# Kernel tuning notes

Hardware: AMD Instinct MI355X
Metric: run time of the kernel (lower is better)

## Reference

```python
import jax, jax.numpy as jnp
import numpy as np

D_STATE = 16

def setup_inputs() -> dict:
    key = jax.random.key(0)
    ks = jax.random.split(key, 7)
    B, L, d_model = 2, 4096, 1024
    d_inner, d_conv, d_state = 2048, 4, D_STATE
    s = 0.02
    return {
        "x": jax.random.normal(ks[0], (B, L, d_model), jnp.float32),
        "W_in": jax.random.normal(ks[1], (2 * d_inner, d_model), jnp.float32) * s,
        "conv_w": jax.random.normal(ks[2], (d_inner, d_conv), jnp.float32) * 0.3,
        "conv_b": jax.random.normal(ks[3], (d_inner,), jnp.float32) * 0.1,
        "W_xproj": jax.random.normal(ks[4], (2 * d_state + d_inner, d_inner), jnp.float32) * s,
        "D": jnp.ones((d_inner,), jnp.float32),
        "W_out": jax.random.normal(ks[5], (d_model, d_inner), jnp.float32) * s,
    }

def _silu(v):
    return v * jax.nn.sigmoid(v)

def reference(x, W_in, conv_w, conv_b, W_xproj, D, W_out):
    Bsz, L, _ = x.shape
    d_inner, d_conv = conv_w.shape
    d_state = D_STATE
    # in_proj -> split into x branch and gate z
    xz = jnp.einsum('bld,ed->ble', x, W_in)           # [B,L,2*d_inner]
    xb, z = xz[..., :d_inner], xz[..., d_inner:]
    # causal depthwise conv1d (left pad d_conv-1, truncate to L)
    xpad = jnp.pad(xb, ((0, 0), (d_conv - 1, 0), (0, 0)))
    xc = conv_b
    for k in range(d_conv):  # tiny fixed kernel loop
        xc = xc + conv_w[:, k] * xpad[:, k:k + L, :]
    xc = _silu(xc)                                    # [B,L,d_inner]
    # x_proj -> B, C, delta
    proj = jnp.einsum('bld,ed->ble', xc, W_xproj)     # [B,L,2*d_state+d_inner]
    Bm = proj[..., :d_state]
    Cm = proj[..., d_state:2 * d_state]
    delta = jax.nn.softplus(proj[..., 2 * d_state:])  # [B,L,d_inner]
    # selective 'scan' as written collapses: y[b,l,d] = delta*x * sum_s B*C + D*x
    bc = jnp.einsum('bls,bls->bl', Bm, Cm)            # [B,L]
    y = delta * xc * bc[..., None] + D * xc
    y = y * _silu(z)
    return jnp.einsum('bld,ed->ble', y, W_out)        # [B,L,d_model]
```

## Files before the change

### kernel.cpp

```cpp
#include <hip/hip_runtime.h>
#include <hip/hip_bf16.h>
#include <cstdint>
#include <cmath>

typedef __bf16 bf16x8 __attribute__((ext_vector_type(8)));
typedef float  f32x4  __attribute__((ext_vector_type(4)));
typedef unsigned short u16x8 __attribute__((ext_vector_type(8)));

#define BT 128
#define BK 64

__device__ __forceinline__ float bf2f(unsigned short h) {
  union { unsigned int u; float f; } v; v.u = ((unsigned int)h) << 16;
  return v.f;
}
__device__ __forceinline__ unsigned short f2bf(float x) {
  union { float f; unsigned int u; } v; v.f = x;
  unsigned int r = v.u + 0x7fffu + ((v.u >> 16) & 1u);
  return (unsigned short)(r >> 16);
}

__device__ __forceinline__ void gld_lds16(const void* g, void* l) {
  __builtin_amdgcn_global_load_lds(
      (const __attribute__((address_space(1))) unsigned int*)g,
      (__attribute__((address_space(3))) unsigned int*)l,
      16, 0, 0);
}

__device__ __forceinline__ void cvt4(const float* __restrict__ in,
                                     unsigned short* __restrict__ out, int i) {
  float4 v = reinterpret_cast<const float4*>(in)[i];
  ushort4 o;
  o.x = f2bf(v.x); o.y = f2bf(v.y); o.z = f2bf(v.z); o.w = f2bf(v.w);
  reinterpret_cast<ushort4*>(out)[i] = o;
}

__global__ void cvt_head(const float* __restrict__ x, unsigned short* __restrict__ xb,
                         const float* __restrict__ W_in, unsigned short* __restrict__ wb) {
  int b = blockIdx.x;
  if (b < 8192) cvt4(x, xb, b * 256 + threadIdx.x);
  else          cvt4(W_in, wb, (b - 8192) * 256 + threadIdx.x);
}

__device__ void conv_strip(const unsigned short* __restrict__ xz,
                           const float* __restrict__ conv_w,
                           const float* __restrict__ conv_b,
                           unsigned short* __restrict__ xc,
                           int strip, int tid) {
  const int bl0  = strip * 32;
  const int seq0 = bl0 & ~4095;
  const int c0   = tid * 8;
  float w[4][8], bb[8];
#pragma unroll
  for (int j = 0; j < 8; ++j) {
    float4 wr = reinterpret_cast<const float4*>(conv_w)[c0 + j];
    w[0][j] = wr.x; w[1][j] = wr.y; w[2][j] = wr.z; w[3][j] = wr.w;
    bb[j] = conv_b[c0 + j];
  }
  float win[3][8];
#pragma unroll
  for (int i = 0; i < 3; ++i) {
    int r = bl0 - 3 + i;
    if (r >= seq0) {
      u16x8 v = *reinterpret_cast<const u16x8*>(xz + (size_t)r * 4096 + c0);
#pragma unroll
      for (int j = 0; j < 8; ++j) win[i][j] = bf2f(v[j]);
    } else {
#pragma unroll
      for (int j = 0; j < 8; ++j) win[i][j] = 0.f;
    }
  }
  for (int i = 0; i < 32; ++i) {
    const int bl = bl0 + i;
    u16x8 v = *reinterpret_cast<const u16x8*>(xz + (size_t)bl * 4096 + c0);
    u16x8 o;
#pragma unroll
    for (int j = 0; j < 8; ++j) {
      float cur = bf2f(v[j]);
      float a = bb[j] + w[0][j] * win[0][j] + w[1][j] * win[1][j]
                      + w[2][j] * win[2][j] + w[3][j] * cur;
      o[j] = f2bf(a / (1.f + __expf(-a)));
      win[0][j] = win[1][j]; win[1][j] = win[2][j]; win[2][j] = cur;
    }
    *reinterpret_cast<u16x8*>(xc + (size_t)bl * 2048 + c0) = o;
  }
}

__global__ void mid_fused(const unsigned short* __restrict__ xz,
                          const float* __restrict__ conv_w,
                          const float* __restrict__ conv_b,
                          unsigned short* __restrict__ xc,
                          const float* __restrict__ W_xproj, unsigned short* __restrict__ wx_bf,
                          const float* __restrict__ W_out,   unsigned short* __restrict__ wo_bf) {
  int b = blockIdx.x;
  if (b < 256) { conv_strip(xz, conv_w, conv_b, xc, b, threadIdx.x); return; }
  b -= 256;
  if (b < 4160) { cvt4(W_xproj, wx_bf, b * 256 + threadIdx.x); return; }
  cvt4(W_out, wo_bf, (b - 4160) * 256 + threadIdx.x);
}

template <int GUARD_N, int OUT_F32>
__global__ __launch_bounds__(256, 2)
void gemm_bt(const unsigned short* __restrict__ A,
             const unsigned short* __restrict__ B,
             void* __restrict__ Cv,
             int N, int K, int ldA, int ldB, int ldC)
{
  __shared__ __align__(16) unsigned short sA[BT * BK];
  __shared__ __align__(16) unsigned short sB[BT * BK];

  const int tid  = threadIdx.x;
  const int lane = tid & 63;
  const int wave = tid >> 6;
  const int row0 = blockIdx.x * BT;
  const int col0 = blockIdx.y * BT;

  const int wrow = (wave & 1) * 64;
  const int wcol = (wave >> 1) * 64;
  const int l15  = lane & 15;
  const int q    = lane >> 4;

  f32x4 acc[4][4];
#pragma unroll
  for (int i = 0; i < 4; ++i)
#pragma unroll
    for (int j = 0; j < 4; ++j)
      acc[i][j] = (f32x4){0.f, 0.f, 0.f, 0.f};

  const int nk = K / BK;
  for (int kt = 0; kt < nk; ++kt) {
    const int k0 = kt * BK;
#pragma unroll
    for (int t = 0; t < 4; ++t) {
      int c  = t * 256 + tid;
      int r  = c >> 3;
      int g  = c & 7;
      int gs = (g ^ (r & 7)) * 8;
      gld_lds16(A + (size_t)(row0 + r) * ldA + k0 + gs, (void*)(sA + c * 8));
      int br = col0 + r;
      if (GUARD_N) br = (br < N) ? br : (N - 1);
      gld_lds16(B + (size_t)br * ldB + k0 + gs, (void*)(sB + c * 8));
    }
    __syncthreads();

#pragma unroll
    for (int kk = 0; kk < BK; kk += 32) {
      const int grb = kk >> 3;
      bf16x8 af[4], bfr[4];
#pragma unroll
      for (int i = 0; i < 4; ++i) {
        int ar = wrow + i * 16 + l15;
        af[i] = *reinterpret_cast<const bf16x8*>(
            sA + ar * BK + (((grb + q) ^ (ar & 7)) << 3));
        int br = wcol + i * 16 + l15;
        bfr[i] = *reinterpret_cast<const bf16x8*>(
            sB + br * BK + (((grb + q) ^ (br & 7)) << 3));
      }
#pragma unroll
      for (int i = 0; i < 4; ++i)
#pragma unroll
        for (int j = 0; j < 4; ++j)
          acc[i][j] = __builtin_amdgcn_mfma_f32_16x16x32_bf16(af[i], bfr[j], acc[i][j], 0, 0, 0);
    }
    __syncthreads();
  }

#pragma unroll
  for (int i = 0; i < 4; ++i) {
#pragma unroll
    for (int j = 0; j < 4; ++j) {
      int colw = col0 + wcol + j * 16 + l15;
      if (GUARD_N && colw >= N) continue;
#pragma unroll
      for (int r = 0; r < 4; ++r) {
        int roww = row0 + wrow + i * 16 + q * 4 + r;
        if (OUT_F32)
          ((float*)Cv)[(size_t)roww * ldC + colw] = acc[i][j][r];
        else
          ((unsigned short*)Cv)[(size_t)roww * ldC + colw] = f2bf(acc[i][j][r]);
      }
    }
  }
}

#define BARX() do { __builtin_amdgcn_sched_barrier(0); \
                    __builtin_amdgcn_s_barrier(); \
                    __builtin_amdgcn_sched_barrier(0); } while (0)
#define VMW(n) asm volatile("s_waitcnt vmcnt(" #n ")" ::: "memory")
#define LGKM0() asm volatile("s_waitcnt lgkmcnt(0)" ::: "memory")

#define STAGE_A(b, h, kt) do { \
  const unsigned short* _p = Ab + (size_t)((h) * 128) * ldA + (kt) * 64; \
  gld_lds16(_p,                     (void*)&sA[b][((h) * 128      + rr) * 64 + (g8 << 3)]); \
  gld_lds16(_p + (size_t)64 * ldA,  (void*)&sA[b][((h) * 128 + 64 + rr) * 64 + (g8 << 3)]); \
} while (0)

#define STAGE_B(b, h, kt) do { \
  const unsigned short* _p = Bb + (size_t)((h) * 128) * ldB + (kt) * 64; \
  gld_lds16(_p,                     (void*)&sB[b][((h) * 128      + rr) * 64 + (g8 << 3)]); \
  gld_lds16(_p + (size_t)64 * ldB,  (void*)&sB[b][((h) * 128 + 64 + rr) * 64 + (g8 << 3)]); \
} while (0)

#define RD_A_SET(dst, b, p) do { \
  dst[0][0] = *reinterpret_cast<const bf16x8*>(&sA[b][aOff + (2*(p)    ) * 1024 + kph0]); \
  dst[0][1] = *reinterpret_cast<const bf16x8*>(&sA[b][aOff + (2*(p)    ) * 1024 + kph1]); \
  dst[1][0] = *reinterpret_cast<const bf16x8*>(&sA[b][aOff + (2*(p) + 1) * 1024 + kph0]); \
  dst[1][1] = *reinterpret_cast<const bf16x8*>(&sA[b][aOff + (2*(p) + 1) * 1024 + kph1]); \
} while (0)

#define RD_B_SET(dst, b) do { \
  dst[0][0] = *reinterpret_cast<const bf16x8*>(&sB[b][bOff + 0 * 1024 + kph0]); \
  dst[0][1] = *reinterpret_cast<const bf16x8*>(&sB[b][bOff + 0 * 1024 + kph1]); \
  dst[1][0] = *reinterpret_cast<const bf16x8*>(&sB[b][bOff + 1 * 1024 + kph0]); \
  dst[1][1] = *reinterpret_cast<const bf16x8*>(&sB[b][bOff + 1 * 1024 + kph1]); \
  dst[2][0] = *reinterpret_cast<const bf16x8*>(&sB[b][bOff + 2 * 1024 + kph0]); \
  dst[2][1] = *reinterpret_cast<const bf16x8*>(&sB[b][bOff + 2 * 1024 + kph1]); \
  dst[3][0] = *reinterpret_cast<const bf16x8*>(&sB[b][bOff + 3 * 1024 + kph0]); \
  dst[3][1] = *reinterpret_cast<const bf16x8*>(&sB[b][bOff + 3 * 1024 + kph1]); \
} while (0)

#define MMA(i, j, k, Af, Bf) \
  acc[i][j] = __builtin_amdgcn_mfma_f32_16x16x32_bf16(Af[(i) & 1][k], Bf[j][k], acc[i][j], 0, 0, 0)

#define MFMA_PH(p, Af, Bf) do { \
  __builtin_amdgcn_s_setprio(1); \
  MMA(2*(p),   0, 0, Af, Bf); MMA(2*(p),   1, 0, Af, Bf); \
  MMA(2*(p),   2, 0, Af, Bf); MMA(2*(p),   3, 0, Af, Bf); \
  MMA(2*(p)+1, 0, 0, Af, Bf); MMA(2*(p)+1, 1, 0, Af, Bf); \
  MMA(2*(p)+1, 2, 0, Af, Bf); MMA(2*(p)+1, 3, 0, Af, Bf); \
  MMA(2*(p),   0, 1, Af, Bf); MMA(2*(p),   1, 1, Af, Bf); \
  MMA(2*(p),   2, 1, Af, Bf); MMA(2*(p),   3, 1, Af, Bf); \
  MMA(2*(p)+1, 0, 1, Af, Bf); MMA(2*(p)+1, 1, 1, Af, Bf); \
  MMA(2*(p)+1, 2, 1, Af, Bf); MMA(2*(p)+1, 3, 1, Af, Bf); \
  __builtin_amdgcn_s_setprio(0); \
} while (0)

__global__ __launch_bounds__(512, 2)
void gemm256(const unsigned short* __restrict__ A,
             const unsigned short* __restrict__ B,
             unsigned short* __restrict__ C,
             int K, int ldA, int ldB, int ldC, int ccsh)
{
  __shared__ __align__(16) unsigned short smem[4 * 256 * 64];
  unsigned short (*sA)[256 * 64] = (unsigned short (*)[256 * 64])smem;
  unsigned short (*sB)[256 * 64] = (unsigned short (*)[256 * 64])(smem + 2 * 256 * 64);

  const int tid  = threadIdx.x;
  const int lane = tid & 63;
  const int wave = tid >> 6;
  const int wm = wave >> 2;
  const int wn = wave & 3;
  const int l15 = lane & 15;
  const int q   = lane >> 4;

  const int nwg = gridDim.x;
  const int wg  = blockIdx.x;
  const int x   = wg & 7;
  const int c   = wg >> 3;
  const int CC  = 1 << ccsh;
  const int R   = (nwg >> 3) >> ccsh;
  const int row0 = ((x >> 1) * R + (c >> ccsh)) * 256;
  const int col0 = ((x & 1) * CC + (c & (CC - 1))) * 256;

  const int rr  = tid >> 3;
  const int g8  = tid & 7;
  const int gsw = ((g8 ^ (rr & 7)) << 3);
  const unsigned short* Ab = A + (size_t)(row0 + rr) * ldA + gsw;
  const unsigned short* Bb = B + (size_t)(col0 + rr) * ldB + gsw;

  const int aOff = (wm * 128 + l15) * 64;
  const int bOff = (wn * 64  + l15) * 64;
  const int a7   = l15 & 7;
  const int kph0 = ((q       ^ a7) << 3);
  const int kph1 = (((4 + q) ^ a7) << 3);

  f32x4 acc[8][4];
#pragma unroll
  for (int i = 0; i < 8; ++i)
#pragma unroll
    for (int j = 0; j < 4; ++j)
      acc[i][j] = (f32x4){0.f, 0.f, 0.f, 0.f};

  bf16x8 afe[2][2], afo[2][2];
  bf16x8 bfe[4][2], bfo[4][2];

  const int nk = K >> 6;
  STAGE_A(0, 0, 0); STAGE_A(0, 1, 0);
  STAGE_B(0, 0, 0); STAGE_B(0, 1, 0);
  STAGE_B(1, 0, 1); STAGE_B(1, 1, 1);
  VMW(4);
  BARX();
  RD_B_SET(bfe, 0); RD_A_SET(afe, 0, 0);

  const int niter = K >> 7;
  for (int it = 0; it < niter; ++it) {
    const int kt1 = 2 * it + 1;
    int ktE = 2 * it + 2; if (ktE > nk - 1) ktE = nk - 1;
    int ktO = 2 * it + 3; if (ktO > nk - 1) ktO = nk - 1;

    STAGE_A(1, 0, kt1);
    BARX();
    MFMA_PH(0, afe, bfe); RD_A_SET(afo, 0, 1);
    BARX();
    STAGE_A(1, 1, kt1);
    BARX();
    MFMA_PH(1, afo, bfe); RD_A_SET(afe, 0, 2);
    BARX();
    STAGE_B(0, 0, ktE);
    BARX();
    MFMA_PH(2, afe, bfe); RD_A_SET(afo, 0, 3);
    BARX();
    STAGE_B(0, 1, ktE);
    VMW(4);
    BARX();
    MFMA_PH(3, afo, bfe); RD_B_SET(bfo, 1); RD_A_SET(afe, 1, 0);
    BARX();

    STAGE_A(0, 0, ktE);
    BARX();
    MFMA_PH(0, afe, bfo); RD_A_SET(afo, 1, 1);
    BARX();
    STAGE_A(0, 1, ktE);
    BARX();
    MFMA_PH(1, afo, bfo); RD_A_SET(afe, 1, 2);
    BARX();
    STAGE_B(1, 0, ktO);
    BARX();
    MFMA_PH(2, afe, bfo); RD_A_SET(afo, 1, 3);
    BARX();
    STAGE_B(1, 1, ktO);
    VMW(4);
    BARX();
    MFMA_PH(3, afo, bfo); RD_B_SET(bfe, 0); RD_A_SET(afe, 0, 0);
    BARX();
  }

  VMW(0);
  LGKM0();
  BARX();
  {
    unsigned short* cs = smem;
#pragma unroll
    for (int i = 0; i < 8; ++i) {
      const int row = wm * 128 + i * 16 + q * 4;
#pragma unroll
      for (int j = 0; j < 4; ++j) {
        const int col = (wn * 64 + j * 16 + l15) ^ (q << 4);
#pragma unroll
        for (int r = 0; r < 4; ++r)
          cs[(row + r) * 256 + col] = f2bf(acc[i][j][r]);
      }
    }
    LGKM0();
    BARX();
#pragma unroll
    for (int s = 0; s < 16; ++s) {
      const int u   = s * 4096 + tid * 8;
      const int row = u >> 8;
      const int col = u & 255;
      const int rcol = col ^ (((row >> 2) & 3) << 4);
      u16x8 v = *reinterpret_cast<const u16x8*>(&cs[row * 256 + rcol]);
      *reinterpret_cast<u16x8*>(C + (size_t)(row0 + row) * ldC + col0 + col) = v;
    }
  }
}

__global__ __launch_bounds__(256)
void proj_strip(const unsigned short* __restrict__ xc,
                const unsigned short* __restrict__ wx,
                unsigned short* __restrict__ proj)
{
  __shared__ float red[4][32 * 32];
  const int tid  = threadIdx.x;
  const int lane = tid & 63;
  const int wave = tid >> 6;
  const int l15  = lane & 15;
  const int q    = lane >> 4;
  const int row0 = blockIdx.x * 32;

  f32x4 acc[2][2];
#pragma unroll
  for (int i = 0; i < 2; ++i)
#pragma unroll
    for (int j = 0; j < 2; ++j) acc[i][j] = (f32x4){0.f, 0.f, 0.f, 0.f};

  const int kbase = wave * 512;
#pragma unroll 4
  for (int kk = 0; kk < 512; kk += 32) {
    const int k = kbase + kk + q * 8;
    bf16x8 a0 = *reinterpret_cast<const bf16x8*>(&xc[(size_t)(row0 + l15) * 2048 + k]);
    bf16x8 a1 = *reinterpret_cast<const bf16x8*>(&xc[(size_t)(row0 + 16 + l15) * 2048 + k]);
    bf16x8 b0 = *reinterpret_cast<const bf16x8*>(&wx[(size_t)(l15) * 2048 + k]);
    bf16x8 b1 = *reinterpret_cast<const bf16x8*>(&wx[(size_t)(16 + l15) * 2048 + k]);
    acc[0][0] = __builtin_amdgcn_mfma_f32_16x16x32_bf16(a0, b0, acc[0][0], 0, 0, 0);
    acc[0][1] = __builtin_amdgcn_mfma_f32_16x16x32_bf16(a0, b1, acc[0][1], 0, 0, 0);
    acc[1][0] = __builtin_amdgcn_mfma_f32_16x16x32_bf16(a1, b0, acc[1][0], 0, 0, 0);
    acc[1][1] = __builtin_amdgcn_mfma_f32_16x16x32_bf16(a1, b1, acc[1][1], 0, 0, 0);
  }

#pragma unroll
  for (int i = 0; i < 2; ++i)
#pragma unroll
    for (int j = 0; j < 2; ++j)
#pragma unroll
      for (int r = 0; r < 4; ++r)
        red[wave][(i * 16 + q * 4 + r) * 32 + j * 16 + l15] = acc[i][j][r];
  __syncthreads();

#pragma unroll
  for (int t = 0; t < 4; ++t) {
    int idx = tid + t * 256;
    float s = red[0][idx] + red[1][idx] + red[2][idx] + red[3][idx];
    proj[(size_t)(row0 + (idx >> 5)) * 2080 + (idx & 31)] = f2bf(s);
  }
}

__global__ void gate_kernel(const unsigned short* __restrict__ proj,
                            const unsigned short* __restrict__ xz,
                            const float* __restrict__ Dw,
                            unsigned short* __restrict__ xc_y)
{
  const int bl = blockIdx.x;
  const unsigned short* p = proj + (size_t)bl * 2080;
  u16x8 pb0 = *reinterpret_cast<const u16x8*>(p);
  u16x8 pb1 = *reinterpret_cast<const u16x8*>(p + 8);
  u16x8 pc0 = *reinterpret_cast<const u16x8*>(p + 16);
  u16x8 pc1 = *reinterpret_cast<const u16x8*>(p + 24);
  float bc = 0.f;
#pragma unroll
  for (int s = 0; s < 8; ++s)
    bc += bf2f(pb0[s]) * bf2f(pc0[s]) + bf2f(pb1[s]) * bf2f(pc1[s]);

  const int c0 = threadIdx.x * 8;
  u16x8 dv  = *reinterpret_cast<const u16x8*>(p + 32 + c0);
  u16x8 xcv = *reinterpret_cast<const u16x8*>(xc_y + (size_t)bl * 2048 + c0);
  u16x8 zv  = *reinterpret_cast<const u16x8*>(xz + (size_t)bl * 4096 + 2048 + c0);
  float4 d0 = reinterpret_cast<const float4*>(Dw)[c0 / 4];
  float4 d1 = reinterpret_cast<const float4*>(Dw)[c0 / 4 + 1];
  const float* dd0 = reinterpret_cast<const float*>(&d0);
  const float* dd1 = reinterpret_cast<const float*>(&d1);

  u16x8 o;
#pragma unroll
  for (int j = 0; j < 8; ++j) {
    float d = bf2f(dv[j]);
    float delta = (d > 15.f) ? d : __logf(1.f + __expf(d));
    float xv = bf2f(xcv[j]);
    float z  = bf2f(zv[j]);
    float Dj = (j < 4) ? dd0[j] : dd1[j - 4];
    float y = delta * xv * bc + Dj * xv;
    y *= z / (1.f + __expf(-z));
    o[j] = f2bf(y);
  }
  *reinterpret_cast<u16x8*>(xc_y + (size_t)bl * 2048 + c0) = o;
}

extern "C" void kernel_launch(void* const* d_in, const int* in_sizes, int n_in,
                              void* d_out, int out_size, void* d_ws, size_t ws_size,
                              hipStream_t stream) {
  const float* x       = (const float*)d_in[0];
  const float* W_in    = (const float*)d_in[1];
  const float* conv_w  = (const float*)d_in[2];
  const float* conv_b  = (const float*)d_in[3];
  const float* W_xproj = (const float*)d_in[4];
  const float* Dw      = (const float*)d_in[5];
  const float* W_out   = (const float*)d_in[6];
  float* out = (float*)d_out;

  unsigned short* xz_bf   = (unsigned short*)d_ws;
  unsigned short* xc_bf   = xz_bf  + (size_t)8192 * 4096;
  unsigned short* proj_bf = xc_bf  + (size_t)8192 * 2048;
  unsigned short* xb_bf   = proj_bf + (size_t)8192 * 2080;
  unsigned short* w_bf    = xb_bf  + (size_t)8192 * 1024;

  cvt_head<<<8192 + 4096, 256, 0, stream>>>(x, xb_bf, W_in, w_bf);
  gemm256<<<512, 512, 0, stream>>>(xb_bf, w_bf, xz_bf, 1024, 1024, 1024, 4096, 3);
  mid_fused<<<256 + 4160 + 2048, 256, 0, stream>>>(xz_bf, conv_w, conv_b, xc_bf,
                                                   W_xproj, xb_bf, W_out, w_bf);
  proj_strip<<<256, 256, 0, stream>>>(xc_bf, xb_bf, proj_bf);
  gemm256<<<256, 512, 0, stream>>>(xc_bf, xb_bf + (size_t)32 * 2048, proj_bf + 32,
                                   2048, 2048, 2048, 2080, 2);
  gate_kernel<<<8192, 256, 0, stream>>>(proj_bf, xz_bf, Dw, xc_bf);
  gemm_bt<0, 1><<<dim3(64, 8), 256, 0, stream>>>(xc_bf, w_bf, out, 1024, 2048, 2048, 2048, 1024);
}
```

Before: 346.3 us.

## Fuse gating epilogue into delta GEMM and reduce B·C inside proj_strip

The elementwise gating kernel is removed. The delta GEMM now computes softplus, the D skip term and the SiLU(z) gate in its epilogue, writing y directly to a new buffer. proj_strip now reduces B·C per row to a single float instead of writing the B and C columns of proj. This drops one kernel launch and the round trip of the full delta matrix through memory, at the cost of a heavier GEMM epilogue that also loads xc, z and bc.

```diff
diff --git a/kernel.cpp b/kernel.cpp
--- a/kernel.cpp
+++ b/kernel.cpp
@@ -235,11 +235,15 @@
   __builtin_amdgcn_s_setprio(0); \
 } while (0)
 
+template <int EPI>
 __global__ __launch_bounds__(512, 2)
 void gemm256(const unsigned short* __restrict__ A,
              const unsigned short* __restrict__ B,
              unsigned short* __restrict__ C,
-             int K, int ldA, int ldB, int ldC, int ccsh)
+             int K, int ldA, int ldB, int ldC, int ccsh,
+             const unsigned short* __restrict__ XZ,
+             const float* __restrict__ Dw,
+             const float* __restrict__ BC)
 {
   __shared__ __align__(16) unsigned short smem[4 * 256 * 64];
   unsigned short (*sA)[256 * 64] = (unsigned short (*)[256 * 64])smem;
@@ -353,14 +357,48 @@
     }
     LGKM0();
     BARX();
-#pragma unroll
-    for (int s = 0; s < 16; ++s) {
-      const int u   = s * 4096 + tid * 8;
-      const int row = u >> 8;
-      const int col = u & 255;
-      const int rcol = col ^ (((row >> 2) & 3) << 4);
-      u16x8 v = *reinterpret_cast<const u16x8*>(&cs[row * 256 + rcol]);
-      *reinterpret_cast<u16x8*>(C + (size_t)(row0 + row) * ldC + col0 + col) = v;
+
+    const int colf   = (tid * 8) & 255;
+    const int rowofs = tid >> 5;
+
+    if (EPI == 0) {
+#pragma unroll
+      for (int s = 0; s < 16; ++s) {
+        const int row  = s * 16 + rowofs;
+        const int rcol = colf ^ (((row >> 2) & 3) << 4);
+        u16x8 v = *reinterpret_cast<const u16x8*>(&cs[row * 256 + rcol]);
+        *reinterpret_cast<u16x8*>(C + (size_t)(row0 + row) * ldC + col0 + colf) = v;
+      }
+    } else {
+      float dj[8];
+      {
+        float4 d0 = reinterpret_cast<const float4*>(Dw)[(col0 + colf) >> 2];
+        float4 d1 = reinterpret_cast<const float4*>(Dw)[((col0 + colf) >> 2) + 1];
+        dj[0] = d0.x; dj[1] = d0.y; dj[2] = d0.z; dj[3] = d0.w;
+        dj[4] = d1.x; dj[5] = d1.y; dj[6] = d1.z; dj[7] = d1.w;
+      }
+#pragma unroll
+      for (int s = 0; s < 16; ++s) {
+        const int row  = s * 16 + rowofs;
+        const int rcol = colf ^ (((row >> 2) & 3) << 4);
+        const size_t gr = (size_t)(row0 + row);
+        u16x8 pv  = *reinterpret_cast<const u16x8*>(&cs[row * 256 + rcol]);
+        u16x8 xcv = *reinterpret_cast<const u16x8*>(A + gr * ldA + col0 + colf);
+        u16x8 zv  = *reinterpret_cast<const u16x8*>(XZ + gr * 4096 + 2048 + col0 + colf);
+        const float bcr = BC[gr];
+        u16x8 o;
+#pragma unroll
+        for (int j = 0; j < 8; ++j) {
+          float p  = bf2f(pv[j]);
+          float delta = (p > 15.f) ? p : __logf(1.f + __expf(p));
+          float xv = bf2f(xcv[j]);
+          float zz = bf2f(zv[j]);
+          float y  = delta * xv * bcr + dj[j] * xv;
+          y *= zz / (1.f + __expf(-zz));
+          o[j] = f2bf(y);
+        }
+        *reinterpret_cast<u16x8*>(C + gr * ldC + col0 + colf) = o;
+      }
     }
   }
 }
@@ -368,9 +406,9 @@
 __global__ __launch_bounds__(256)
 void proj_strip(const unsigned short* __restrict__ xc,
                 const unsigned short* __restrict__ wx,
-                unsigned short* __restrict__ proj)
+                float* __restrict__ bc)
 {
-  __shared__ float red[4][32 * 32];
+  __shared__ float red[4][32 * 33];
   const int tid  = threadIdx.x;
   const int lane = tid & 63;
   const int wave = tid >> 6;
@@ -404,55 +442,20 @@
     for (int j = 0; j < 2; ++j)
 #pragma unroll
       for (int r = 0; r < 4; ++r)
-        red[wave][(i * 16 + q * 4 + r) * 32 + j * 16 + l15] = acc[i][j][r];
+        red[wave][(i * 16 + q * 4 + r) * 33 + j * 16 + l15] = acc[i][j][r];
   __syncthreads();
 
-#pragma unroll
-  for (int t = 0; t < 4; ++t) {
-    int idx = tid + t * 256;
-    float s = red[0][idx] + red[1][idx] + red[2][idx] + red[3][idx];
-    proj[(size_t)(row0 + (idx >> 5)) * 2080 + (idx & 31)] = f2bf(s);
-  }
-}
-
-__global__ void gate_kernel(const unsigned short* __restrict__ proj,
-                            const unsigned short* __restrict__ xz,
-                            const float* __restrict__ Dw,
-                            unsigned short* __restrict__ xc_y)
-{
-  const int bl = blockIdx.x;
-  const unsigned short* p = proj + (size_t)bl * 2080;
-  u16x8 pb0 = *reinterpret_cast<const u16x8*>(p);
-  u16x8 pb1 = *reinterpret_cast<const u16x8*>(p + 8);
-  u16x8 pc0 = *reinterpret_cast<const u16x8*>(p + 16);
-  u16x8 pc1 = *reinterpret_cast<const u16x8*>(p + 24);
-  float bc = 0.f;
-#pragma unroll
-  for (int s = 0; s < 8; ++s)
-    bc += bf2f(pb0[s]) * bf2f(pc0[s]) + bf2f(pb1[s]) * bf2f(pc1[s]);
-
-  const int c0 = threadIdx.x * 8;
-  u16x8 dv  = *reinterpret_cast<const u16x8*>(p + 32 + c0);
-  u16x8 xcv = *reinterpret_cast<const u16x8*>(xc_y + (size_t)bl * 2048 + c0);
-  u16x8 zv  = *reinterpret_cast<const u16x8*>(xz + (size_t)bl * 4096 + 2048 + c0);
-  float4 d0 = reinterpret_cast<const float4*>(Dw)[c0 / 4];
-  float4 d1 = reinterpret_cast<const float4*>(Dw)[c0 / 4 + 1];
-  const float* dd0 = reinterpret_cast<const float*>(&d0);
-  const float* dd1 = reinterpret_cast<const float*>(&d1);
-
-  u16x8 o;
-#pragma unroll
-  for (int j = 0; j < 8; ++j) {
-    float d = bf2f(dv[j]);
-    float delta = (d > 15.f) ? d : __logf(1.f + __expf(d));
-    float xv = bf2f(xcv[j]);
-    float z  = bf2f(zv[j]);
-    float Dj = (j < 4) ? dd0[j] : dd1[j - 4];
-    float y = delta * xv * bc + Dj * xv;
-    y *= z / (1.f + __expf(-z));
-    o[j] = f2bf(y);
-  }
-  *reinterpret_cast<u16x8*>(xc_y + (size_t)bl * 2048 + c0) = o;
+  if (tid < 32) {
+    float s = 0.f;
+#pragma unroll
+    for (int cc = 0; cc < 16; ++cc) {
+      const int ib = tid * 33 + cc;
+      float b  = red[0][ib] + red[1][ib] + red[2][ib] + red[3][ib];
+      float cv = red[0][ib + 16] + red[1][ib + 16] + red[2][ib + 16] + red[3][ib + 16];
+      s += b * cv;
+    }
+    bc[row0 + tid] = s;
+  }
 }
 
 extern "C" void kernel_launch(void* const* d_in, const int* in_sizes, int n_in,
@@ -469,17 +472,19 @@
 
   unsigned short* xz_bf   = (unsigned short*)d_ws;
   unsigned short* xc_bf   = xz_bf  + (size_t)8192 * 4096;
-  unsigned short* proj_bf = xc_bf  + (size_t)8192 * 2048;
-  unsigned short* xb_bf   = proj_bf + (size_t)8192 * 2080;
+  unsigned short* y_bf    = xc_bf  + (size_t)8192 * 2048;
+  float*          bc_ws   = (float*)(y_bf + (size_t)8192 * 2048);
+  unsigned short* xb_bf   = y_bf + (size_t)8192 * 2080;
   unsigned short* w_bf    = xb_bf  + (size_t)8192 * 1024;
 
   cvt_head<<<8192 + 4096, 256, 0, stream>>>(x, xb_bf, W_in, w_bf);
-  gemm256<<<512, 512, 0, stream>>>(xb_bf, w_bf, xz_bf, 1024, 1024, 1024, 4096, 3);
+  gemm256<0><<<512, 512, 0, stream>>>(xb_bf, w_bf, xz_bf, 1024, 1024, 1024, 4096, 3,
+                                      nullptr, nullptr, nullptr);
   mid_fused<<<256 + 4160 + 2048, 256, 0, stream>>>(xz_bf, conv_w, conv_b, xc_bf,
                                                    W_xproj, xb_bf, W_out, w_bf);
-  proj_strip<<<256, 256, 0, stream>>>(xc_bf, xb_bf, proj_bf);
-  gemm256<<<256, 512, 0, stream>>>(xc_bf, xb_bf + (size_t)32 * 2048, proj_bf + 32,
-                                   2048, 2048, 2048, 2080, 2);
-  gate_kernel<<<8192, 256, 0, stream>>>(proj_bf, xz_bf, Dw, xc_bf);
-  gemm_bt<0, 1><<<dim3(64, 8), 256, 0, stream>>>(xc_bf, w_bf, out, 1024, 2048, 2048, 2048, 1024);
-}
+  proj_strip<<<256, 256, 0, stream>>>(xc_bf, xb_bf, bc_ws);
+  gemm256<1><<<256, 512, 0, stream>>>(xc_bf, xb_bf + (size_t)32 * 2048, y_bf,
+                                      2048, 2048, 2048, 2048, 2,
+                                      xz_bf, Dw, bc_ws);
+  gemm_bt<0, 1><<<dim3(64, 8), 256, 0, stream>>>(y_bf, w_bf, out, 1024, 2048, 2048, 2048, 1024);
+}
```

After: 338.9 us. -2.1%, faster.
